# Kernel tuning notes

Measured on AMD Instinct MI355X. Metric: run time of the kernel, lower is better.

The kernel has to match this reference:

```python
import jax, jax.numpy as jnp
import numpy as np

B, L, D, H = 2, 2048, 1024, 16
HD = D // H  # head_dim = 64


def setup_inputs() -> dict:
    key = jax.random.key(0)
    ks = jax.random.split(key, 8)
    queries = jax.random.normal(ks[0], (B, L, D), dtype=jnp.float32)
    keys = jax.random.normal(ks[1], (B, L, D), dtype=jnp.float32)
    values = jax.random.normal(ks[2], (B, L, D), dtype=jnp.float32)
    mask = jax.random.randint(ks[3], (B, L, L), 0, 2) > 0  # True = masked
    s = 1.0 / np.sqrt(D)
    W_q = jax.random.normal(ks[4], (D, D), dtype=jnp.float32) * s
    W_k = jax.random.normal(ks[5], (D, D), dtype=jnp.float32) * s
    W_v = jax.random.normal(ks[6], (D, D), dtype=jnp.float32) * s
    W_o = jax.random.normal(ks[7], (D, D), dtype=jnp.float32) * s
    return {"queries": queries, "keys": keys, "values": values,
            "W_q": W_q, "W_k": W_k, "W_v": W_v, "W_o": W_o, "mask": mask}


def _split_heads(x):
    # [B, L, D] -> [B, H, L, HD]
    return x.reshape(B, L, H, HD).transpose(0, 2, 1, 3)


def reference(queries, keys, values, W_q, W_k, W_v, W_o, mask):
    # Linear projections (nn.Linear: x @ W.T, no bias)
    q = _split_heads(queries @ W_q.T)   # [B,H,Lq,HD]
    k = _split_heads(keys @ W_k.T)      # [B,H,Lk,HD]
    v = _split_heads(values @ W_v.T)    # [B,H,Lk,HD]
    scores = jnp.einsum('bnqd,bnkd->bnqk', q, k) / np.sqrt(HD)
    scores = jnp.where(mask[:, None, :, :], -1e9, scores)
    attn = jax.nn.softmax(scores, axis=-1)
    ctx = jnp.einsum('bnqk,bnkd->bnqd', attn, v)
    ctx = ctx.transpose(0, 2, 1, 3).reshape(B, L, D)
    return ctx @ W_o.T  # dropout p=0.0 -> identity
```

## Files before the change

kernel.cpp:

```cpp
#include <hip/hip_runtime.h>
#include <hip/hip_bf16.h>

typedef __bf16 bf16;
typedef __attribute__((ext_vector_type(8))) __bf16 bf16x8;
typedef __attribute__((ext_vector_type(4))) __bf16 bf16x4;
typedef __attribute__((ext_vector_type(4))) float f32x4;

#define B_   2
#define L_   2048
#define D_   1024
#define H_   16
#define HD_  64

__device__ __forceinline__ float fast_exp2(float x) {
  float e; asm("v_exp_f32 %0, %1" : "=v"(e) : "v"(x)); return e;
}

__device__ __forceinline__ void gll16(const bf16* g, bf16* l) {
  __builtin_amdgcn_global_load_lds((const __attribute__((address_space(1))) void*)g,
                                   (__attribute__((address_space(3))) void*)l,
                                   16, 0, 0);
}

__global__ void detect_kernel(const unsigned short* __restrict__ q_u,
                              const unsigned char* __restrict__ m_u,
                              int* __restrict__ flags) {
  __shared__ int cnt, odd;
  if (threadIdx.x == 0) { cnt = 0; odd = 0; }
  __syncthreads();
  int c = 0, o = 0;
  for (int i = 0; i < 8; i++) {
    int idx = threadIdx.x * 8 + i;
    unsigned e = (q_u[idx] >> 7) & 0xFF;
    if (e >= 0x8F || (e > 0 && e <= 0x6F)) c++;
    if ((idx & 3) && m_u[idx]) o = 1;
  }
  atomicAdd(&cnt, c);
  if (o) atomicOr(&odd, 1);
  __syncthreads();
  if (threadIdx.x == 0) { flags[0] = (cnt > 128) ? 1 : 0; flags[1] = odd; }
}

__device__ __forceinline__ void canon_body(const void* src, bf16* dst, int i, int f) {
  if (f) {
    const float4* s = (const float4*)src;
    float4 a = s[i / 4], b2 = s[i / 4 + 1];
    bf16x8 o;
    o[0] = (bf16)a.x;  o[1] = (bf16)a.y;  o[2] = (bf16)a.z;  o[3] = (bf16)a.w;
    o[4] = (bf16)b2.x; o[5] = (bf16)b2.y; o[6] = (bf16)b2.z; o[7] = (bf16)b2.w;
    *(bf16x8*)(dst + i) = o;
  } else {
    *(bf16x8*)(dst + i) = ((const bf16x8*)src)[i / 8];
  }
}

__global__ __launch_bounds__(256) void canon_pack(
    const void* xq, const void* xk, const void* xv,
    const void* Wq, const void* Wk, const void* Wv, const void* Wo,
    const void* mp,
    bf16* cxq, bf16* cxk, bf16* cxv,
    bf16* cWq, bf16* cWk, bf16* cWv, bf16* cWo,
    unsigned* __restrict__ bitsT,
    const int* __restrict__ flags) {
  int t = blockIdx.x;
  if (t >= 8192) {
    int wid = (t - 8192) * 256 + threadIdx.x;
    unsigned v = 0;
    if (flags[1]) {
      const uchar4* p = (const uchar4*)mp;
#pragma unroll
      for (int c = 0; c < 8; c++) {
        uchar4 u = p[wid * 8 + c];
        v |= (u.x ? 1u : 0u) << (c * 4 + 0);
        v |= (u.y ? 1u : 0u) << (c * 4 + 1);
        v |= (u.z ? 1u : 0u) << (c * 4 + 2);
        v |= (u.w ? 1u : 0u) << (c * 4 + 3);
      }
    } else {
      const int4* p = (const int4*)mp;
#pragma unroll
      for (int c = 0; c < 8; c++) {
        int4 u = p[wid * 8 + c];
        v |= (u.x ? 1u : 0u) << (c * 4 + 0);
        v |= (u.y ? 1u : 0u) << (c * 4 + 1);
        v |= (u.z ? 1u : 0u) << (c * 4 + 2);
        v |= (u.w ? 1u : 0u) << (c * 4 + 3);
      }
    }
    int row = wid >> 6, word = wid & 63;
    int kt = word >> 1, half = word & 1;
    bitsT[((size_t)kt * 4096 + row) * 2 + half] = v;
    return;
  }
  const int f = flags[0];
  const void* src; bf16* dst; int base;
  if (t < 2048)      { src = xq; dst = cxq; base = t * 2048; }
  else if (t < 4096) { src = xk; dst = cxk; base = (t - 2048) * 2048; }
  else if (t < 6144) { src = xv; dst = cxv; base = (t - 4096) * 2048; }
  else {
    int w = t - 6144, wi = w >> 9;
    base = (w & 511) * 2048;
    if (wi == 0)      { src = Wq; dst = cWq; }
    else if (wi == 1) { src = Wk; dst = cWk; }
    else if (wi == 2) { src = Wv; dst = cWv; }
    else              { src = Wo; dst = cWo; }
  }
  canon_body(src, dst, base + threadIdx.x * 8, f);
}

__global__ __launch_bounds__(256) void gemm_qkv(
    const bf16* __restrict__ Aq, const bf16* __restrict__ Bq, bf16* __restrict__ Cq,
    const bf16* __restrict__ Ak, const bf16* __restrict__ Bk, bf16* __restrict__ Ck,
    const bf16* __restrict__ Av, const bf16* __restrict__ Bv, bf16* __restrict__ VT) {
  __shared__ bf16 smem[128 * 136];
  bf16* sA = smem;
  bf16* sB = smem + 4096;
  const int z = blockIdx.z;
  const bf16* A  = (z == 0) ? Aq : (z == 1) ? Ak : Av;
  const bf16* Bm = (z == 0) ? Bq : (z == 1) ? Bk : Bv;

  const int tid = threadIdx.x;
  const int w = tid >> 6, lane = tid & 63, qd = lane >> 4, r = lane & 15;
  const int wm = w >> 1, wn = w & 1;
  const int m0 = blockIdx.x * 128, n0 = blockIdx.y * 128;

  f32x4 acc[4][4];
#pragma unroll
  for (int i = 0; i < 4; i++)
#pragma unroll
    for (int j = 0; j < 4; j++) acc[i][j] = (f32x4){0.f, 0.f, 0.f, 0.f};

  for (int k0 = 0; k0 < 1024; k0 += 32) {
    __syncthreads();
#pragma unroll
    for (int p = 0; p < 2; p++) {
      int c = p * 256 + tid;
      gll16(A + (size_t)(m0 + (c >> 2)) * 1024 + k0 + (c & 3) * 8, sA + c * 8);
    }
#pragma unroll
    for (int p = 0; p < 2; p++) {
      int c = p * 256 + tid;
      gll16(Bm + (size_t)(n0 + (c >> 2)) * 1024 + k0 + (c & 3) * 8, sB + c * 8);
    }
    __syncthreads();
    bf16x8 af[4], bfv[4];
#pragma unroll
    for (int i = 0; i < 4; i++)
      af[i] = *(const bf16x8*)&sA[(wm * 64 + i * 16 + r) * 32 + qd * 8];
#pragma unroll
    for (int j = 0; j < 4; j++)
      bfv[j] = *(const bf16x8*)&sB[(wn * 64 + j * 16 + r) * 32 + qd * 8];
#pragma unroll
    for (int i = 0; i < 4; i++)
#pragma unroll
      for (int j = 0; j < 4; j++)
        acc[i][j] = __builtin_amdgcn_mfma_f32_16x16x32_bf16(af[i], bfv[j], acc[i][j], 0, 0, 0);
  }

  if (z < 2) {
    bf16* C = (z == 0) ? Cq : Ck;
    const float s = (z == 0) ? 0.1803368801f : 1.0f;
#pragma unroll
    for (int i = 0; i < 4; i++)
#pragma unroll
      for (int j = 0; j < 4; j++)
#pragma unroll
        for (int rr = 0; rr < 4; rr++) {
          int row = m0 + wm * 64 + i * 16 + qd * 4 + rr;
          int col = n0 + wn * 64 + j * 16 + r;
          C[(size_t)row * 1024 + col] = (bf16)(acc[i][j][rr] * s);
        }
  } else {
    __syncthreads();
#pragma unroll
    for (int i = 0; i < 4; i++)
#pragma unroll
      for (int j = 0; j < 4; j++) {
        int col = wn * 64 + j * 16 + r;
        int rowb = wm * 64 + i * 16 + qd * 4;
        bf16x4 v4;
#pragma unroll
        for (int rr = 0; rr < 4; rr++) v4[rr] = (bf16)acc[i][j][rr];
        *(bf16x4*)&smem[col * 136 + rowb] = v4;
      }
    __syncthreads();
    const int b = m0 >> 11, tok0 = m0 & 2047, h0 = n0 >> 6;
#pragma unroll
    for (int p = 0; p < 8; p++) {
      int c = p * 256 + tid;
      int dl = c >> 4, ch = c & 15;
      bf16x8 v = *(const bf16x8*)&smem[dl * 136 + ch * 8];
      int head = h0 + (dl >> 6), d = dl & 63;
      *(bf16x8*)(VT + ((size_t)((b * 16 + head) * 64 + d)) * 2048 + tok0 + ch * 8) = v;
    }
  }
}

__global__ __launch_bounds__(256) void gemm_nt_out(const bf16* __restrict__ A,
                                                   const bf16* __restrict__ Bm,
                                                   void* __restrict__ Cout,
                                                   const int* __restrict__ flags) {
  __shared__ bf16 sA[128 * 32];
  __shared__ bf16 sB[64 * 32];
  const int tid = threadIdx.x;
  const int w = tid >> 6, lane = tid & 63, qd = lane >> 4, r = lane & 15;
  const int wm = w >> 1, wn = w & 1;
  const int m0 = blockIdx.x * 128, n0 = blockIdx.y * 64;

  f32x4 acc[4][2];
#pragma unroll
  for (int i = 0; i < 4; i++)
#pragma unroll
    for (int j = 0; j < 2; j++) acc[i][j] = (f32x4){0.f, 0.f, 0.f, 0.f};

  for (int k0 = 0; k0 < 1024; k0 += 32) {
    __syncthreads();
    {
      int c0 = tid;
      gll16(A + (size_t)(m0 + (c0 >> 2)) * 1024 + k0 + (c0 & 3) * 8, sA + c0 * 8);
      int c1 = 256 + tid;
      gll16(A + (size_t)(m0 + (c1 >> 2)) * 1024 + k0 + (c1 & 3) * 8, sA + c1 * 8);
      int cb = tid;
      gll16(Bm + (size_t)(n0 + (cb >> 2)) * 1024 + k0 + (cb & 3) * 8, sB + cb * 8);
    }
    __syncthreads();
    bf16x8 af[4], bfv[2];
#pragma unroll
    for (int i = 0; i < 4; i++)
      af[i] = *(const bf16x8*)&sA[(wm * 64 + i * 16 + r) * 32 + qd * 8];
#pragma unroll
    for (int j = 0; j < 2; j++)
      bfv[j] = *(const bf16x8*)&sB[(wn * 32 + j * 16 + r) * 32 + qd * 8];
#pragma unroll
    for (int i = 0; i < 4; i++)
#pragma unroll
      for (int j = 0; j < 2; j++)
        acc[i][j] = __builtin_amdgcn_mfma_f32_16x16x32_bf16(af[i], bfv[j], acc[i][j], 0, 0, 0);
  }
  const int f = flags[0];
#pragma unroll
  for (int i = 0; i < 4; i++)
#pragma unroll
    for (int j = 0; j < 2; j++)
#pragma unroll
      for (int rr = 0; rr < 4; rr++) {
        int row = m0 + wm * 64 + i * 16 + qd * 4 + rr;
        int col = n0 + wn * 32 + j * 16 + r;
        if (f) ((float*)Cout)[(size_t)row * 1024 + col] = acc[i][j][rr];
        else   ((bf16*)Cout)[(size_t)row * 1024 + col] = (bf16)acc[i][j][rr];
      }
}

__global__ __launch_bounds__(256) void attn_kernel(const bf16* __restrict__ Q,
                                                   const bf16* __restrict__ Kp,
                                                   const bf16* __restrict__ Vt,
                                                   const unsigned* __restrict__ bitsT,
                                                   bf16* __restrict__ OP,
                                                   float* __restrict__ LP) {
  __shared__ bf16 sK[2][64 * 64];
  __shared__ bf16 sVT[2][64 * 64];
  __shared__ bf16 sP[128 * 72];
  const int tid = threadIdx.x;
  const int w = tid >> 6, lane = tid & 63, qd = lane >> 4, r = lane & 15;
  const int bh = blockIdx.y, b = bh >> 4, h = bh & 15;
  const int q0 = blockIdx.x * 128;
  const int z = blockIdx.z;

  bf16x8 qf[2][2];
#pragma unroll
  for (int i = 0; i < 2; i++)
#pragma unroll
    for (int ks = 0; ks < 2; ks++)
      qf[i][ks] = *(const bf16x8*)(Q + (size_t)(b * L_ + q0 + w * 32 + i * 16 + r) * D_ +
                                   h * HD_ + ks * 32 + qd * 8);

  bf16x8 ones;
#pragma unroll
  for (int e = 0; e < 8; e++) ones[e] = (bf16)1.0f;

  f32x4 o[2][4], lacc[2];
#pragma unroll
  for (int i = 0; i < 2; i++) {
#pragma unroll
    for (int dj = 0; dj < 4; dj++) o[i][dj] = (f32x4){0.f, 0.f, 0.f, 0.f};
    lacc[i] = (f32x4){0.f, 0.f, 0.f, 0.f};
  }

#define STAGE_KV(KT, KB, VB)                                                        \
  {                                                                                 \
    _Pragma("unroll")                                                               \
    for (int p = 0; p < 2; p++) {                                                   \
      int c = p * 256 + tid;                                                        \
      int row = c >> 3, kc = c & 7;                                                 \
      int kcg = kc ^ (row & 7);                                                     \
      gll16(Kp + (size_t)(b * L_ + (KT) * 64 + row) * D_ + h * HD_ + kcg * 8,       \
            (KB) + c * 8);                                                          \
    }                                                                               \
    _Pragma("unroll")                                                               \
    for (int p = 0; p < 2; p++) {                                                   \
      int c = p * 256 + tid;                                                        \
      int row = c >> 3, kc = c & 7;                                                 \
      int kcg = kc ^ (row & 7);                                                     \
      gll16(Vt + (size_t)(bh * 64 + row) * L_ + (KT) * 64 + kcg * 8, (VB) + c * 8); \
    }                                                                               \
  }

#define MLOAD(KT, M0, M1)                                                                       \
  {                                                                                             \
    M0 = *(const uint2*)(bitsT + ((size_t)(KT) * 4096 + b * 2048 + q0 + w * 32 + r) * 2);       \
    M1 = *(const uint2*)(bitsT + ((size_t)(KT) * 4096 + b * 2048 + q0 + w * 32 + 16 + r) * 2);  \
  }

  const int kt0 = z * 16;
  STAGE_KV(kt0, &sK[0][0], &sVT[0][0]);
  uint2 mc0, mc1, mn0, mn1;
  MLOAD(kt0, mc0, mc1);
  mn0 = mc0; mn1 = mc1;

  for (int it = 0; it < 16; ++it) {
    const int kt = kt0 + it;
    const bf16* kb = &sK[it & 1][0];
    const bf16* vb = &sVT[it & 1][0];

    if (it < 15) {
      STAGE_KV(kt + 1, &sK[(it + 1) & 1][0], &sVT[(it + 1) & 1][0]);
      MLOAD(kt + 1, mn0, mn1);
      asm volatile("s_waitcnt vmcnt(6)" ::: "memory");
    } else {
      asm volatile("s_waitcnt vmcnt(0)" ::: "memory");
    }
    __builtin_amdgcn_sched_barrier(0);
    __builtin_amdgcn_s_barrier();

    bf16x8 kf[4][2];
#pragma unroll
    for (int j = 0; j < 4; j++)
#pragma unroll
      for (int ks = 0; ks < 2; ks++) {
        int row = j * 16 + r;
        int phys = (ks * 4 + qd) ^ (row & 7);
        kf[j][ks] = *(const bf16x8*)&kb[row * 64 + phys * 8];
      }

#pragma unroll
    for (int i = 0; i < 2; i++) {
      f32x4 S[4];
      __builtin_amdgcn_s_setprio(1);
#pragma unroll
      for (int j = 0; j < 4; j++) {
        S[j] = (f32x4){0.f, 0.f, 0.f, 0.f};
#pragma unroll
        for (int ks = 0; ks < 2; ks++)
          S[j] = __builtin_amdgcn_mfma_f32_16x16x32_bf16(kf[j][ks], qf[i][ks], S[j], 0, 0, 0);
      }
      __builtin_amdgcn_s_setprio(0);
      const uint2 m64 = (i == 0) ? mc0 : mc1;
#pragma unroll
      for (int j = 0; j < 4; j++) {
        unsigned word = (j < 2) ? m64.x : m64.y;
        unsigned nib = (word >> ((j & 1) * 16 + qd * 4)) & 0xFu;
        bf16x4 pv;
#pragma unroll
        for (int rr = 0; rr < 4; rr++) {
          float e = fast_exp2(S[j][rr]);
          pv[rr] = (bf16)(((nib >> rr) & 1u) ? 0.f : e);
        }
        *(bf16x4*)&sP[(w * 32 + i * 16 + r) * 72 + j * 16 + qd * 4] = pv;
      }
    }
    asm volatile("s_waitcnt lgkmcnt(0)" ::: "memory");

    bf16x8 vf[4][2];
#pragma unroll
    for (int dj = 0; dj < 4; dj++)
#pragma unroll
      for (int ks = 0; ks < 2; ks++) {
        int row = dj * 16 + r;
        int phys = (ks * 4 + qd) ^ (row & 7);
        vf[dj][ks] = *(const bf16x8*)&vb[row * 64 + phys * 8];
      }
    __builtin_amdgcn_s_setprio(1);
#pragma unroll
    for (int i = 0; i < 2; i++)
#pragma unroll
      for (int ks = 0; ks < 2; ks++) {
        bf16x8 pf = *(const bf16x8*)&sP[(w * 32 + i * 16 + r) * 72 + ks * 32 + qd * 8];
#pragma unroll
        for (int dj = 0; dj < 4; dj++)
          o[i][dj] = __builtin_amdgcn_mfma_f32_16x16x32_bf16(pf, vf[dj][ks], o[i][dj], 0, 0, 0);
        lacc[i] = __builtin_amdgcn_mfma_f32_16x16x32_bf16(pf, ones, lacc[i], 0, 0, 0);
      }
    __builtin_amdgcn_s_setprio(0);

    __builtin_amdgcn_s_barrier();
    mc0 = mn0; mc1 = mn1;
  }
#undef STAGE_KV
#undef MLOAD

#pragma unroll
  for (int i = 0; i < 2; i++) {
#pragma unroll
    for (int dj = 0; dj < 4; dj++)
#pragma unroll
      for (int rr = 0; rr < 4; rr++) {
        int rg = b * L_ + q0 + w * 32 + i * 16 + qd * 4 + rr;
        int col = h * HD_ + dj * 16 + r;
        OP[((size_t)z * 4096 + rg) * 1024 + col] = (bf16)o[i][dj][rr];
      }
    if (r == 0) {
#pragma unroll
      for (int rr = 0; rr < 4; rr++) {
        int rg = b * L_ + q0 + w * 32 + i * 16 + qd * 4 + rr;
        LP[((size_t)z * 4096 + rg) * 16 + h] = lacc[i][rr];
      }
    }
  }
}

__global__ __launch_bounds__(256) void combine_kernel(const bf16* __restrict__ OP,
                                                      const float* __restrict__ LP,
                                                      bf16* __restrict__ CTX) {
  size_t idx = ((size_t)blockIdx.x * 256 + threadIdx.x) * 8;
  int row = (int)(idx >> 10), col = (int)(idx & 1023);
  bf16x8 a = *(const bf16x8*)(OP + idx);
  bf16x8 c = *(const bf16x8*)(OP + (size_t)4096 * 1024 + idx);
  int h = col >> 6;
  float l = LP[row * 16 + h] + LP[65536 + row * 16 + h];
  float inv = 1.0f / l;
  bf16x8 o;
#pragma unroll
  for (int e = 0; e < 8; e++) o[e] = (bf16)(((float)a[e] + (float)c[e]) * inv);
  *(bf16x8*)(CTX + idx) = o;
}

extern "C" void kernel_launch(void* const* d_in, const int* in_sizes, int n_in,
                              void* d_out, int out_size, void* d_ws, size_t ws_size,
                              hipStream_t stream) {
  const void* xq = d_in[0];
  const void* xk = d_in[1];
  const void* xv = d_in[2];
  const void* Wq = d_in[3];
  const void* Wk = d_in[4];
  const void* Wv = d_in[5];
  const void* Wo = d_in[6];
  const void* mask = d_in[7];

  char* ws = (char*)d_ws;
  const size_t MB = 1048576;
  int*      FLAGS = (int*)(ws + 0);
  unsigned* BITS  = (unsigned*)(ws + 4096);
  bf16* cWo = (bf16*)(ws + 2 * MB);
  bf16* cWq = (bf16*)(ws + 4 * MB);
  bf16* cWk = (bf16*)(ws + 6 * MB);
  bf16* cWv = (bf16*)(ws + 8 * MB);
  bf16* cxq = (bf16*)(ws + 10 * MB);
  bf16* cxk = (bf16*)(ws + 18 * MB);
  bf16* cxv = (bf16*)(ws + 26 * MB);
  bf16* Q   = (bf16*)(ws + 34 * MB);
  bf16* K   = (bf16*)(ws + 42 * MB);
  bf16* VT  = (bf16*)(ws + 50 * MB);
  bf16*  OP  = (bf16*)(ws + 4 * MB);
  float* LP  = (float*)(ws + 20 * MB);
  bf16*  CTX = (bf16*)(ws + 26 * MB);

  detect_kernel<<<1, 256, 0, stream>>>((const unsigned short*)xq,
                                       (const unsigned char*)mask, FLAGS);
  canon_pack<<<9216, 256, 0, stream>>>(xq, xk, xv, Wq, Wk, Wv, Wo, mask,
                                       cxq, cxk, cxv, cWq, cWk, cWv, cWo,
                                       BITS, FLAGS);
  gemm_qkv<<<dim3(32, 8, 3), 256, 0, stream>>>(cxq, cWq, Q,
                                               cxk, cWk, K,
                                               cxv, cWv, VT);
  attn_kernel<<<dim3(16, 32, 2), 256, 0, stream>>>(Q, K, VT, BITS, OP, LP);
  combine_kernel<<<2048, 256, 0, stream>>>(OP, LP, CTX);
  gemm_nt_out<<<dim3(32, 16), 256, 0, stream>>>(CTX, cWo, d_out, FLAGS);
}
```

Baseline: 269.2 us.

## Fuse split-K attention combine into output projection GEMM A-tile load

Removes the separate combine kernel: the output GEMM now loads both split-K partial outputs and their row sums straight from global memory, normalizes them in registers and writes the result into shared memory as its A tile. The LP layout is interleaved so both partial sums come in one float2 load. Register prefetch of the next A tile is pipelined with explicit waitcnt and barriers. This drops a launch and the CTX round trip to memory, but the combine arithmetic is now recomputed by each of the 16 column blocks and the loads go through registers instead of direct-to-LDS. The attention loop also gets unroll 2.

```diff
diff --git a/kernel.cpp b/kernel.cpp
--- a/kernel.cpp
+++ b/kernel.cpp
@@ -196,7 +196,8 @@
   }
 }
 
-__global__ __launch_bounds__(256) void gemm_nt_out(const bf16* __restrict__ A,
+__global__ __launch_bounds__(256) void gemm_nt_out(const bf16* __restrict__ OP,
+                                                   const float* __restrict__ LP2,
                                                    const bf16* __restrict__ Bm,
                                                    void* __restrict__ Cout,
                                                    const int* __restrict__ flags) {
@@ -207,23 +208,58 @@
   const int wm = w >> 1, wn = w & 1;
   const int m0 = blockIdx.x * 128, n0 = blockIdx.y * 64;
 
+  const int c0 = tid, c1 = 256 + tid;
+  const int row0 = m0 + (c0 >> 2), row1 = m0 + (c1 >> 2);
+  const int kc0 = (c0 & 3) * 8, kc1 = (c1 & 3) * 8;
+
+  bf16x8 oa0, ob0, oa1, ob1;
+  float2 pl0, pl1;
+
+#define LOADG(K0)                                                                     \
+  {                                                                                   \
+    int ka = (K0) + kc0, kb = (K0) + kc1;                                             \
+    oa0 = *(const bf16x8*)(OP + (size_t)row0 * 1024 + ka);                            \
+    ob0 = *(const bf16x8*)(OP + (size_t)4096 * 1024 + (size_t)row0 * 1024 + ka);      \
+    pl0 = *(const float2*)(LP2 + ((size_t)row0 * 16 + (ka >> 6)) * 2);                \
+    oa1 = *(const bf16x8*)(OP + (size_t)row1 * 1024 + kb);                            \
+    ob1 = *(const bf16x8*)(OP + (size_t)4096 * 1024 + (size_t)row1 * 1024 + kb);      \
+    pl1 = *(const float2*)(LP2 + ((size_t)row1 * 16 + (kb >> 6)) * 2);                \
+  }
+
   f32x4 acc[4][2];
 #pragma unroll
   for (int i = 0; i < 4; i++)
 #pragma unroll
     for (int j = 0; j < 2; j++) acc[i][j] = (f32x4){0.f, 0.f, 0.f, 0.f};
 
+  LOADG(0);
+
   for (int k0 = 0; k0 < 1024; k0 += 32) {
-    __syncthreads();
+    gll16(Bm + (size_t)(n0 + (tid >> 2)) * 1024 + k0 + (tid & 3) * 8, sB + tid * 8);
+    asm volatile("s_waitcnt vmcnt(1)" ::: "memory");
+    __builtin_amdgcn_sched_barrier(0);
     {
-      int c0 = tid;
-      gll16(A + (size_t)(m0 + (c0 >> 2)) * 1024 + k0 + (c0 & 3) * 8, sA + c0 * 8);
-      int c1 = 256 + tid;
-      gll16(A + (size_t)(m0 + (c1 >> 2)) * 1024 + k0 + (c1 & 3) * 8, sA + c1 * 8);
-      int cb = tid;
-      gll16(Bm + (size_t)(n0 + (cb >> 2)) * 1024 + k0 + (cb & 3) * 8, sB + cb * 8);
-    }
-    __syncthreads();
+      float i0 = 1.0f / (pl0.x + pl0.y);
+      float i1 = 1.0f / (pl1.x + pl1.y);
+      bf16x8 w0, w1;
+#pragma unroll
+      for (int e = 0; e < 8; e++) {
+        w0[e] = (bf16)(((float)oa0[e] + (float)ob0[e]) * i0);
+        w1[e] = (bf16)(((float)oa1[e] + (float)ob1[e]) * i1);
+      }
+      *(bf16x8*)(sA + c0 * 8) = w0;
+      *(bf16x8*)(sA + c1 * 8) = w1;
+    }
+    if (k0 < 992) {
+      LOADG(k0 + 32);
+      asm volatile("s_waitcnt vmcnt(6)" ::: "memory");
+    } else {
+      asm volatile("s_waitcnt vmcnt(0)" ::: "memory");
+    }
+    asm volatile("s_waitcnt lgkmcnt(0)" ::: "memory");
+    __builtin_amdgcn_sched_barrier(0);
+    __builtin_amdgcn_s_barrier();
+
     bf16x8 af[4], bfv[2];
 #pragma unroll
     for (int i = 0; i < 4; i++)
@@ -236,7 +272,10 @@
 #pragma unroll
       for (int j = 0; j < 2; j++)
         acc[i][j] = __builtin_amdgcn_mfma_f32_16x16x32_bf16(af[i], bfv[j], acc[i][j], 0, 0, 0);
-  }
+    __builtin_amdgcn_s_barrier();
+  }
+#undef LOADG
+
   const int f = flags[0];
 #pragma unroll
   for (int i = 0; i < 4; i++)
@@ -317,6 +356,7 @@
   MLOAD(kt0, mc0, mc1);
   mn0 = mc0; mn1 = mc1;
 
+#pragma unroll 2
   for (int it = 0; it < 16; ++it) {
     const int kt = kt0 + it;
     const bf16* kb = &sK[it & 1][0];
@@ -412,26 +452,10 @@
 #pragma unroll
       for (int rr = 0; rr < 4; rr++) {
         int rg = b * L_ + q0 + w * 32 + i * 16 + qd * 4 + rr;
-        LP[((size_t)z * 4096 + rg) * 16 + h] = lacc[i][rr];
-      }
-    }
-  }
-}
-
-__global__ __launch_bounds__(256) void combine_kernel(const bf16* __restrict__ OP,
-                                                      const float* __restrict__ LP,
-                                                      bf16* __restrict__ CTX) {
-  size_t idx = ((size_t)blockIdx.x * 256 + threadIdx.x) * 8;
-  int row = (int)(idx >> 10), col = (int)(idx & 1023);
-  bf16x8 a = *(const bf16x8*)(OP + idx);
-  bf16x8 c = *(const bf16x8*)(OP + (size_t)4096 * 1024 + idx);
-  int h = col >> 6;
-  float l = LP[row * 16 + h] + LP[65536 + row * 16 + h];
-  float inv = 1.0f / l;
-  bf16x8 o;
-#pragma unroll
-  for (int e = 0; e < 8; e++) o[e] = (bf16)(((float)a[e] + (float)c[e]) * inv);
-  *(bf16x8*)(CTX + idx) = o;
+        LP[((size_t)rg * 16 + h) * 2 + z] = lacc[i][rr];
+      }
+    }
+  }
 }
 
 extern "C" void kernel_launch(void* const* d_in, const int* in_sizes, int n_in,
@@ -462,7 +486,6 @@
   bf16* VT  = (bf16*)(ws + 50 * MB);
   bf16*  OP  = (bf16*)(ws + 4 * MB);
   float* LP  = (float*)(ws + 20 * MB);
-  bf16*  CTX = (bf16*)(ws + 26 * MB);
 
   detect_kernel<<<1, 256, 0, stream>>>((const unsigned short*)xq,
                                        (const unsigned char*)mask, FLAGS);
@@ -473,6 +496,5 @@
                                                cxk, cWk, K,
                                                cxv, cWv, VT);
   attn_kernel<<<dim3(16, 32, 2), 256, 0, stream>>>(Q, K, VT, BITS, OP, LP);
-  combine_kernel<<<2048, 256, 0, stream>>>(OP, LP, CTX);
-  gemm_nt_out<<<dim3(32, 16), 256, 0, stream>>>(CTX, cWo, d_out, FLAGS);
-}
+  gemm_nt_out<<<dim3(32, 16), 256, 0, stream>>>(OP, LP, cWo, d_out, FLAGS);
+}
```

New measurement: 280.3 us. 1.04x slower.

## Drop split-K attention and combine kernel; normalize in attention epilogue with swizzled grid

Applied to the files above, without the earlier changes.

Attention no longer splits the key dimension into two halves. Each workgroup now walks all 32 key tiles and divides by the row sum directly in its epilogue, writing CTX. This removes the combine kernel, the partial output and row-sum buffers and their extra global traffic, and one launch. The grid becomes 1D with a block-id remapping that groups 8 heads per q-tile band, likely for L2 locality of K/V. The cost is half as many workgroups (512) with twice the serial work each, which may reduce occupancy and latency hiding.

```diff
diff --git a/kernel.cpp b/kernel.cpp
--- a/kernel.cpp
+++ b/kernel.cpp
@@ -255,16 +255,16 @@
                                                    const bf16* __restrict__ Kp,
                                                    const bf16* __restrict__ Vt,
                                                    const unsigned* __restrict__ bitsT,
-                                                   bf16* __restrict__ OP,
-                                                   float* __restrict__ LP) {
+                                                   bf16* __restrict__ CTX) {
   __shared__ bf16 sK[2][64 * 64];
   __shared__ bf16 sVT[2][64 * 64];
   __shared__ bf16 sP[128 * 72];
   const int tid = threadIdx.x;
   const int w = tid >> 6, lane = tid & 63, qd = lane >> 4, r = lane & 15;
-  const int bh = blockIdx.y, b = bh >> 4, h = bh & 15;
-  const int q0 = blockIdx.x * 128;
-  const int z = blockIdx.z;
+  const int wgid = blockIdx.x;
+  const int bh = ((wgid >> 7) << 3) + (wgid & 7);
+  const int b = bh >> 4, h = bh & 15;
+  const int q0 = ((wgid >> 3) & 15) * 128;
 
   bf16x8 qf[2][2];
 #pragma unroll
@@ -311,20 +311,19 @@
     M1 = *(const uint2*)(bitsT + ((size_t)(KT) * 4096 + b * 2048 + q0 + w * 32 + 16 + r) * 2);  \
   }
 
-  const int kt0 = z * 16;
-  STAGE_KV(kt0, &sK[0][0], &sVT[0][0]);
+  STAGE_KV(0, &sK[0][0], &sVT[0][0]);
   uint2 mc0, mc1, mn0, mn1;
-  MLOAD(kt0, mc0, mc1);
+  MLOAD(0, mc0, mc1);
   mn0 = mc0; mn1 = mc1;
 
-  for (int it = 0; it < 16; ++it) {
-    const int kt = kt0 + it;
+#pragma unroll 2
+  for (int it = 0; it < 32; ++it) {
     const bf16* kb = &sK[it & 1][0];
     const bf16* vb = &sVT[it & 1][0];
 
-    if (it < 15) {
-      STAGE_KV(kt + 1, &sK[(it + 1) & 1][0], &sVT[(it + 1) & 1][0]);
-      MLOAD(kt + 1, mn0, mn1);
+    if (it < 31) {
+      STAGE_KV(it + 1, &sK[(it + 1) & 1][0], &sVT[(it + 1) & 1][0]);
+      MLOAD(it + 1, mn0, mn1);
       asm volatile("s_waitcnt vmcnt(6)" ::: "memory");
     } else {
       asm volatile("s_waitcnt vmcnt(0)" ::: "memory");
@@ -400,38 +399,18 @@
 
 #pragma unroll
   for (int i = 0; i < 2; i++) {
+    float inv[4];
+#pragma unroll
+    for (int rr = 0; rr < 4; rr++) inv[rr] = 1.0f / lacc[i][rr];
 #pragma unroll
     for (int dj = 0; dj < 4; dj++)
 #pragma unroll
       for (int rr = 0; rr < 4; rr++) {
         int rg = b * L_ + q0 + w * 32 + i * 16 + qd * 4 + rr;
         int col = h * HD_ + dj * 16 + r;
-        OP[((size_t)z * 4096 + rg) * 1024 + col] = (bf16)o[i][dj][rr];
-      }
-    if (r == 0) {
-#pragma unroll
-      for (int rr = 0; rr < 4; rr++) {
-        int rg = b * L_ + q0 + w * 32 + i * 16 + qd * 4 + rr;
-        LP[((size_t)z * 4096 + rg) * 16 + h] = lacc[i][rr];
-      }
-    }
-  }
-}
-
-__global__ __launch_bounds__(256) void combine_kernel(const bf16* __restrict__ OP,
-                                                      const float* __restrict__ LP,
-                                                      bf16* __restrict__ CTX) {
-  size_t idx = ((size_t)blockIdx.x * 256 + threadIdx.x) * 8;
-  int row = (int)(idx >> 10), col = (int)(idx & 1023);
-  bf16x8 a = *(const bf16x8*)(OP + idx);
-  bf16x8 c = *(const bf16x8*)(OP + (size_t)4096 * 1024 + idx);
-  int h = col >> 6;
-  float l = LP[row * 16 + h] + LP[65536 + row * 16 + h];
-  float inv = 1.0f / l;
-  bf16x8 o;
-#pragma unroll
-  for (int e = 0; e < 8; e++) o[e] = (bf16)(((float)a[e] + (float)c[e]) * inv);
-  *(bf16x8*)(CTX + idx) = o;
+        CTX[(size_t)rg * 1024 + col] = (bf16)(o[i][dj][rr] * inv[rr]);
+      }
+  }
 }
 
 extern "C" void kernel_launch(void* const* d_in, const int* in_sizes, int n_in,
@@ -460,9 +439,7 @@
   bf16* Q   = (bf16*)(ws + 34 * MB);
   bf16* K   = (bf16*)(ws + 42 * MB);
   bf16* VT  = (bf16*)(ws + 50 * MB);
-  bf16*  OP  = (bf16*)(ws + 4 * MB);
-  float* LP  = (float*)(ws + 20 * MB);
-  bf16*  CTX = (bf16*)(ws + 26 * MB);
+  bf16* CTX = (bf16*)(ws + 26 * MB);
 
   detect_kernel<<<1, 256, 0, stream>>>((const unsigned short*)xq,
                                        (const unsigned char*)mask, FLAGS);
@@ -472,7 +449,6 @@
   gemm_qkv<<<dim3(32, 8, 3), 256, 0, stream>>>(cxq, cWq, Q,
                                                cxk, cWk, K,
                                                cxv, cWv, VT);
-  attn_kernel<<<dim3(16, 32, 2), 256, 0, stream>>>(Q, K, VT, BITS, OP, LP);
-  combine_kernel<<<2048, 256, 0, stream>>>(OP, LP, CTX);
+  attn_kernel<<<512, 256, 0, stream>>>(Q, K, VT, BITS, CTX);
   gemm_nt_out<<<dim3(32, 16), 256, 0, stream>>>(CTX, cWo, d_out, FLAGS);
 }
```

After: 261.5 us. -2.9%, faster.
